# Optimization experiments

Hardware: AMD Instinct MI355X
Metric: run time of the kernel (lower is better)

The kernel has to match this reference:

```python
import jax, jax.numpy as jnp
import numpy as np

HIDDEN = 2048
N_HEADS = 16
N_KV = 4
HEAD_DIM = 128
SEQ = 2048
BATCH = 2
THETA = 10000.0


def rotate_half(x):
    half = x.shape[-1] // 2
    x1, x2 = x[..., :half], x[..., half:]
    return jnp.concatenate((-x2, x1), axis=-1)


def rope_cos_sin(seq_len, dim, theta, dtype):
    inv_freq = 1.0 / (theta ** (jnp.arange(0, dim, 2, dtype=jnp.float32) / dim))
    t = jnp.arange(seq_len, dtype=jnp.float32)
    freqs = jnp.einsum('i,j->ij', t, inv_freq)            # [S, dim/2]
    emb = jnp.concatenate((freqs, freqs), axis=-1)        # [S, dim]
    return jnp.cos(emb).astype(dtype), jnp.sin(emb).astype(dtype)


def setup_inputs() -> dict:
    key = jax.random.key(0)
    kx, kq, kk, kv, ko = jax.random.split(key, 5)
    s = 0.02
    return {
        'x':  jax.random.normal(kx, (BATCH, SEQ, HIDDEN), dtype=jnp.float32),
        'Wq': jax.random.normal(kq, (HIDDEN, N_HEADS * HEAD_DIM), dtype=jnp.float32) * s,
        'Wk': jax.random.normal(kk, (HIDDEN, N_KV * HEAD_DIM), dtype=jnp.float32) * s,
        'Wv': jax.random.normal(kv, (HIDDEN, N_KV * HEAD_DIM), dtype=jnp.float32) * s,
        'Wo': jax.random.normal(ko, (N_HEADS * HEAD_DIM, HIDDEN), dtype=jnp.float32) * s,
    }


def reference(x, Wq, Wk, Wv, Wo):
    B, S, _ = x.shape
    q = (x @ Wq).reshape(B, S, N_HEADS, HEAD_DIM)
    k = (x @ Wk).reshape(B, S, N_KV, HEAD_DIM)
    v = (x @ Wv).reshape(B, S, N_KV, HEAD_DIM)

    cos, sin = rope_cos_sin(S, HEAD_DIM, THETA, x.dtype)
    cos = cos[None, :, None, :]  # [1,S,1,D]
    sin = sin[None, :, None, :]
    q = q * cos + rotate_half(q) * sin
    k = k * cos + rotate_half(k) * sin

    repeat = N_HEADS // N_KV
    k = jnp.repeat(k, repeat, axis=2)  # repeat_interleave over heads
    v = jnp.repeat(v, repeat, axis=2)

    # [B,H,S,D]
    q = q.transpose(0, 2, 1, 3)
    k = k.transpose(0, 2, 1, 3)
    v = v.transpose(0, 2, 1, 3)

    scale = HEAD_DIM ** -0.5
    scores = jnp.einsum('bhqd,bhkd->bhqk', q, k) * scale
    causal = jnp.triu(jnp.full((S, S), -jnp.inf, dtype=scores.dtype), k=1)
    scores = scores + causal
    probs = jax.nn.softmax(scores, axis=-1)
    out = jnp.einsum('bhqk,bhkd->bhqd', probs, v)
    out = out.transpose(0, 2, 1, 3).reshape(B, S, N_HEADS * HEAD_DIM)
    return out @ Wo
```

## Files before the change

### kernel.cpp

```cpp
#include <hip/hip_runtime.h>
#include <hip/hip_bf16.h>
#include <math.h>

#define HIDDEN 2048
#define NHEADS 16
#define NKV 4
#define HD 128
#define SEQ 2048
#define BATCH 2
#define MTOT (BATCH*SEQ)
#define NQ (NHEADS*HD)
#define NKVD (NKV*HD)
#define NQKV (NQ + 2*NKVD)

typedef __attribute__((ext_vector_type(8))) short short8;
typedef __attribute__((ext_vector_type(4))) float float4v;

#if __has_builtin(__builtin_amdgcn_exp2f)
#define EXP2F __builtin_amdgcn_exp2f
#else
#define EXP2F exp2f
#endif
#define C1 0.1275174f

static __device__ __forceinline__ unsigned short f2bf(float f) {
  union { float f; unsigned int u; } v; v.f = f;
  unsigned int r = v.u + 0x7FFF + ((v.u >> 16) & 1);
  return (unsigned short)(r >> 16);
}
static __device__ __forceinline__ float bf2f(unsigned short h) {
  union { unsigned int u; float f; } v; v.u = ((unsigned int)h) << 16;
  return v.f;
}

static __device__ __forceinline__ void async16(const unsigned short* g, unsigned short* l) {
  __builtin_amdgcn_global_load_lds(
      (const __attribute__((address_space(1))) unsigned int*)g,
      (__attribute__((address_space(3))) unsigned int*)l, 16, 0, 0);
}

__global__ void cast_f32_bf16(const float* __restrict__ in,
                              unsigned short* __restrict__ out, int n) {
  int i = (blockIdx.x * blockDim.x + threadIdx.x) * 4;
  if (i < n) {
    float4 v = *(const float4*)(in + i);
    ushort4 o;
    o.x = f2bf(v.x); o.y = f2bf(v.y); o.z = f2bf(v.z); o.w = f2bf(v.w);
    *(ushort4*)(out + i) = o;
  }
}

__global__ void transpose_cast(const float* __restrict__ W,
                               unsigned short* __restrict__ Wt, int K, int N) {
  __shared__ float tile[32][33];
  int tn = blockIdx.x * 32;
  int tk = blockIdx.y * 32;
  int tx = threadIdx.x & 31;
  int ty = threadIdx.x >> 5;
  #pragma unroll
  for (int i = 0; i < 4; i++) {
    int k = tk + ty + i * 8;
    tile[ty + i * 8][tx] = W[(size_t)k * N + tn + tx];
  }
  __syncthreads();
  #pragma unroll
  for (int i = 0; i < 4; i++) {
    int n = tn + ty + i * 8;
    Wt[(size_t)n * K + tk + tx] = f2bf(tile[tx][ty + i * 8]);
  }
}

__global__ void rope_kernel(unsigned short* __restrict__ Qb, int nheads) {
  int idx = blockIdx.x * blockDim.x + threadIdx.x;
  int d = idx & 63;
  int hr = idx >> 6;
  int spos = (hr / nheads) % SEQ;
  size_t base = (size_t)hr * HD;
  float inv = exp2f((float)d * -0.2076205059304601f);
  float ang = (float)spos * inv;
  float sn, cs;
  sincosf(ang, &sn, &cs);
  float q1 = bf2f(Qb[base + d]);
  float q2 = bf2f(Qb[base + d + 64]);
  Qb[base + d]      = f2bf(q1 * cs - q2 * sn);
  Qb[base + d + 64] = f2bf(q2 * cs + q1 * sn);
}

__global__ __launch_bounds__(256) void gemm_qkv(
    const unsigned short* __restrict__ A,
    const unsigned short* __restrict__ Bt,
    unsigned short* __restrict__ Qb,
    unsigned short* __restrict__ Kb,
    unsigned short* __restrict__ Vt) {
  __shared__ unsigned short As0[128 * 32], Bs0[128 * 32];
  __shared__ unsigned short As1[128 * 32], Bs1[128 * 32];
  const int K = HIDDEN;
  int bm = blockIdx.y * 128, bn = blockIdx.x * 128;
  int tid = threadIdx.x, w = tid >> 6, lane = tid & 63;
  int wm = (w >> 1) * 64, wn = (w & 1) * 64;
  int m16 = lane & 15, quad = lane >> 4;
  int lrow = lane >> 2, lch = lane & 3;
  const unsigned short* Ag = A + (size_t)(bm + w * 32 + lrow) * K + lch * 8;
  const unsigned short* Bg = Bt + (size_t)(bn + w * 32 + lrow) * K + lch * 8;
  int woff = w * 1024;

  float4v acc[4][4];
  #pragma unroll
  for (int i = 0; i < 4; i++)
    #pragma unroll
    for (int j = 0; j < 4; j++) acc[i][j] = (float4v)0.0f;

  auto stage = [&](int k0, unsigned short* Asl, unsigned short* Bsl) {
    #pragma unroll
    for (int i = 0; i < 2; i++) {
      async16(Ag + (size_t)i * 16 * K + k0, Asl + woff + i * 512);
      async16(Bg + (size_t)i * 16 * K + k0, Bsl + woff + i * 512);
    }
  };
  auto compute = [&](const unsigned short* As, const unsigned short* Bs) {
    short8 af[4], bfr[4];
    #pragma unroll
    for (int i = 0; i < 4; i++)
      af[i] = *(const short8*)(&As[(wm + i * 16 + m16) * 32 + quad * 8]);
    #pragma unroll
    for (int j = 0; j < 4; j++)
      bfr[j] = *(const short8*)(&Bs[(wn + j * 16 + m16) * 32 + quad * 8]);
    #pragma unroll
    for (int i = 0; i < 4; i++)
      #pragma unroll
      for (int j = 0; j < 4; j++)
        acc[i][j] = __builtin_amdgcn_mfma_f32_16x16x32_bf16(af[i], bfr[j], acc[i][j], 0, 0, 0);
  };

  stage(0, As0, Bs0);
  for (int k0 = 0; k0 < K; k0 += 64) {
    __syncthreads();
    if (k0 + 32 < K) stage(k0 + 32, As1, Bs1);
    compute(As0, Bs0);
    __syncthreads();
    if (k0 + 64 < K) stage(k0 + 64, As0, Bs0);
    compute(As1, Bs1);
  }

  if (blockIdx.x < 16) {
    #pragma unroll
    for (int i = 0; i < 4; i++)
      #pragma unroll
      for (int j = 0; j < 4; j++)
        #pragma unroll
        for (int r = 0; r < 4; r++) {
          int row = bm + wm + i * 16 + quad * 4 + r;
          int col = bn + wn + j * 16 + m16;
          Qb[(size_t)row * NQ + col] = f2bf(acc[i][j][r]);
        }
  } else if (blockIdx.x < 20) {
    #pragma unroll
    for (int i = 0; i < 4; i++)
      #pragma unroll
      for (int j = 0; j < 4; j++)
        #pragma unroll
        for (int r = 0; r < 4; r++) {
          int row = bm + wm + i * 16 + quad * 4 + r;
          int col = bn - 2048 + wn + j * 16 + m16;
          Kb[(size_t)row * NKVD + col] = f2bf(acc[i][j][r]);
        }
  } else {
    #pragma unroll
    for (int i = 0; i < 4; i++)
      #pragma unroll
      for (int j = 0; j < 4; j++) {
        int f = bn - 2560 + wn + j * 16 + m16;
        int row0 = bm + wm + i * 16 + quad * 4;
        uint2 u;
        u.x = ((unsigned)f2bf(acc[i][j][1]) << 16) | f2bf(acc[i][j][0]);
        u.y = ((unsigned)f2bf(acc[i][j][3]) << 16) | f2bf(acc[i][j][2]);
        *(uint2*)(Vt + (size_t)f * MTOT + row0) = u;
      }
  }
}

__global__ __launch_bounds__(256) void gemm_o(
    const unsigned short* __restrict__ A,
    const unsigned short* __restrict__ Bt,
    float* __restrict__ C, int M, int N, int K) {
  __shared__ unsigned short As0[128 * 32], Bs0[128 * 32];
  __shared__ unsigned short As1[128 * 32], Bs1[128 * 32];
  int bm = blockIdx.y * 128, bn = blockIdx.x * 128;
  int tid = threadIdx.x, w = tid >> 6, lane = tid & 63;
  int wm = (w >> 1) * 64, wn = (w & 1) * 64;
  int m16 = lane & 15, quad = lane >> 4;
  int lrow = lane >> 2, lch = lane & 3;
  const unsigned short* Ag = A + (size_t)(bm + w * 32 + lrow) * K + lch * 8;
  const unsigned short* Bg = Bt + (size_t)(bn + w * 32 + lrow) * K + lch * 8;
  int woff = w * 1024;

  float4v acc[4][4];
  #pragma unroll
  for (int i = 0; i < 4; i++)
    #pragma unroll
    for (int j = 0; j < 4; j++) acc[i][j] = (float4v)0.0f;

  auto stage = [&](int k0, unsigned short* Asl, unsigned short* Bsl) {
    #pragma unroll
    for (int i = 0; i < 2; i++) {
      async16(Ag + (size_t)i * 16 * K + k0, Asl + woff + i * 512);
      async16(Bg + (size_t)i * 16 * K + k0, Bsl + woff + i * 512);
    }
  };
  auto compute = [&](const unsigned short* As, const unsigned short* Bs) {
    short8 af[4], bfr[4];
    #pragma unroll
    for (int i = 0; i < 4; i++)
      af[i] = *(const short8*)(&As[(wm + i * 16 + m16) * 32 + quad * 8]);
    #pragma unroll
    for (int j = 0; j < 4; j++)
      bfr[j] = *(const short8*)(&Bs[(wn + j * 16 + m16) * 32 + quad * 8]);
    #pragma unroll
    for (int i = 0; i < 4; i++)
      #pragma unroll
      for (int j = 0; j < 4; j++)
        acc[i][j] = __builtin_amdgcn_mfma_f32_16x16x32_bf16(af[i], bfr[j], acc[i][j], 0, 0, 0);
  };

  stage(0, As0, Bs0);
  for (int k0 = 0; k0 < K; k0 += 64) {
    __syncthreads();
    if (k0 + 32 < K) stage(k0 + 32, As1, Bs1);
    compute(As0, Bs0);
    __syncthreads();
    if (k0 + 64 < K) stage(k0 + 64, As0, Bs0);
    compute(As1, Bs1);
  }

  #pragma unroll
  for (int i = 0; i < 4; i++)
    #pragma unroll
    for (int j = 0; j < 4; j++)
      #pragma unroll
      for (int r = 0; r < 4; r++) {
        int row = bm + wm + i * 16 + quad * 4 + r;
        int col = bn + wn + j * 16 + m16;
        C[(size_t)row * N + col] = acc[i][j][r];
      }
}

#define FLASH_TILE(CUR, NXT)                                                  \
  {                                                                           \
    const int ktb = kt * 64;                                                  \
    __syncthreads();           \
    {                                                                         \
      const unsigned short* Vg = Vt + vgrow * (size_t)MTOT                    \
                                    + (size_t)b * SEQ + ktb + kcv * 32 + lch * 8; \
      unsigned short* Vl = Vs + kcv * 4096 + ipv * 512;                       \
      _Pragma("unroll")                                                       \
      for (int i = 0; i < 4; i++) async16(Vg + (size_t)i * 16 * MTOT, Vl + i * 512); \
    }                                                                         \
    const bool act = (ktb <= wqmax);                                          \
    float4v sacc[2][4];                                                       \
    if (act) {                                                                \
      _Pragma("unroll") for (int qs = 0; qs < 2; qs++)                        \
        _Pragma("unroll") for (int s4 = 0; s4 < 4; s4++) sacc[qs][s4] = (float4v)0.0f; \
      _Pragma("unroll")                                                       \
      for (int s4 = 0; s4 < 4; s4++)                                          \
        _Pragma("unroll")                                                     \
        for (int c = 0; c < 4; c++) {                                         \
          short8 kf = *(const short8*)(&CUR[c * 2048 + (s4 * 16 + m16) * 32 + quad * 8]); \
          sacc[0][s4] = __builtin_amdgcn_mfma_f32_16x16x32_bf16(kf, qf[0][c], sacc[0][s4], 0, 0, 0); \
          sacc[1][s4] = __builtin_amdgcn_mfma_f32_16x16x32_bf16(kf, qf[1][c], sacc[1][s4], 0, 0, 0); \
        }                                                                     \
    }                                                                         \
    if (kt < H) {                                                             \
      const unsigned short* Kg = Kp + (((size_t)b * SEQ + (kt + 1) * 64 + lrow) * NKV + kvh) * HD + w * 32 + lch * 8; \
      unsigned short* Kl = NXT + w * 2048;                                    \
      _Pragma("unroll")                                                       \
      for (int i = 0; i < 4; i++) async16(Kg + (size_t)i * 16 * NKV * HD, Kl + i * 512); \
    }                                                                         \
    if (act) {                                                                \
      _Pragma("unroll")                                                       \
      for (int qs = 0; qs < 2; qs++) {                                        \
        const int qabs = wqbase + qs * 16 + m16;                              \
        const bool diag = (ktb + 63) > (wqbase + qs * 16);                    \
        float sv[4][4]; float mloc = -1e30f;                                  \
        if (diag) {                                                           \
          _Pragma("unroll") for (int s4 = 0; s4 < 4; s4++)                    \
            _Pragma("unroll") for (int r = 0; r < 4; r++) {                   \
              int kabs = ktb + s4 * 16 + quad * 4 + r;                        \
              float t = sacc[qs][s4][r];                                      \
              sv[s4][r] = (kabs > qabs) ? -1e30f : t;                         \
              mloc = fmaxf(mloc, sv[s4][r]); }                                \
        } else {                                                              \
          _Pragma("unroll") for (int s4 = 0; s4 < 4; s4++)                    \
            _Pragma("unroll") for (int r = 0; r < 4; r++) {                   \
              sv[s4][r] = sacc[qs][s4][r]; mloc = fmaxf(mloc, sv[s4][r]); }   \
        }                                                                     \
        mloc *= C1;                                                           \
        mloc = fmaxf(mloc, __shfl_xor(mloc, 16, 64));                         \
        mloc = fmaxf(mloc, __shfl_xor(mloc, 32, 64));                         \
        const float mnewS = fmaxf(miS[qs], mloc);                             \
        float pr[4][4]; float rs = 0.0f;                                      \
        _Pragma("unroll") for (int s4 = 0; s4 < 4; s4++)                      \
          _Pragma("unroll") for (int r = 0; r < 4; r++) {                     \
            float p = EXP2F(__builtin_fmaf(sv[s4][r], C1, -mnewS));           \
            pr[s4][r] = p; rs += p; }                                         \
        rs += __shfl_xor(rs, 16, 64);                                         \
        rs += __shfl_xor(rs, 32, 64);                                         \
        const float alpha = EXP2F(miS[qs] - mnewS);                           \
        li[qs] = li[qs] * alpha + rs; miS[qs] = mnewS;                        \
        _Pragma("unroll") for (int ds = 0; ds < 8; ds++) oacc[ds][qs] *= alpha; \
        const int prow = qlocal0 + qs * 16 + m16;                             \
        const int psw = prow * 32; const int rx = prow & 7;                   \
        _Pragma("unroll") for (int s4 = 0; s4 < 4; s4++) {                    \
          uint2 u;                                                            \
          u.x = (__float_as_uint(pr[s4][1]) & 0xffff0000u) | (__float_as_uint(pr[s4][0]) >> 16); \
          u.y = (__float_as_uint(pr[s4][3]) & 0xffff0000u) | (__float_as_uint(pr[s4][2]) >> 16); \
          int chunkW = s4 * 2 + (quad >> 1);                                  \
          *(uint2*)(&Ps[psw + ((chunkW ^ rx) << 2) + (quad & 1) * 2]) = u;    \
        }                                                                     \
      }                                                                       \
    }                                                                         \
    __syncthreads();     \
    if (act) {                                                                \
      const int r0 = qlocal0 + m16, r1 = qlocal0 + 16 + m16;                  \
      _Pragma("unroll")                                                       \
      for (int kc = 0; kc < 2; kc++) {                                        \
        short8 pf0 = *(const short8*)(&Ps[r0 * 32 + (((kc * 4 + quad) ^ (r0 & 7)) << 2)]); \
        short8 pf1 = *(const short8*)(&Ps[r1 * 32 + (((kc * 4 + quad) ^ (r1 & 7)) << 2)]); \
        _Pragma("unroll")                                                     \
        for (int ds = 0; ds < 8; ds++) {                                      \
          short8 vf = *(const short8*)(&Vs[kc * 4096 + (ds * 16 + m16) * 32 + quad * 8]); \
          oacc[ds][0] = __builtin_amdgcn_mfma_f32_16x16x32_bf16(vf, pf0, oacc[ds][0], 0, 0, 0); \
          oacc[ds][1] = __builtin_amdgcn_mfma_f32_16x16x32_bf16(vf, pf1, oacc[ds][1], 0, 0, 0); \
        }                                                                     \
      }                                                                       \
    }                                                                         \
  }

__global__ __launch_bounds__(256, 2) void flash_attn(
    const unsigned short* __restrict__ Q,
    const unsigned short* __restrict__ Kp,
    const unsigned short* __restrict__ Vt,
    unsigned short* __restrict__ O) {
  __shared__ unsigned short Ks0[4 * 64 * 32];
  __shared__ unsigned short Ks1[4 * 64 * 32];
  __shared__ unsigned short Vs[2 * 128 * 32];
  __shared__ unsigned int   Ps[128 * 32];

  int bx = blockIdx.x;
  int h  = blockIdx.y;
  int b  = blockIdx.z;
  int kvh = h >> 2;
  int H = 31 - bx, L = bx;
  int tid = threadIdx.x;
  int w = tid >> 6, lane = tid & 63;
  int m16 = lane & 15, quad = lane >> 4;
  int lrow = lane >> 2, lch = lane & 3;

  int wqbase = (w < 2) ? (H * 64 + w * 32) : (L * 64 + (w - 2) * 32);
  int wqmax = wqbase + 31;
  int qlocal0 = w * 32;
  const int kcv = w >> 1, ipv = (w & 1) * 4;
  const size_t vgrow = (size_t)kvh * HD + ipv * 16 + lrow;

  short8 qf[2][4];
  #pragma unroll
  for (int qs = 0; qs < 2; qs++) {
    size_t qbase = (((size_t)b * SEQ + wqbase + qs * 16 + m16) * NHEADS + h) * HD;
    #pragma unroll
    for (int c = 0; c < 4; c++)
      qf[qs][c] = *(const short8*)(Q + qbase + c * 32 + quad * 8);
  }

  float4v oacc[8][2];
  #pragma unroll
  for (int ds = 0; ds < 8; ds++) { oacc[ds][0] = (float4v)0.0f; oacc[ds][1] = (float4v)0.0f; }
  float miS[2] = {-1e30f, -1e30f}, li[2] = {0.0f, 0.0f};

  {
    const unsigned short* Kg = Kp + (((size_t)b * SEQ + lrow) * NKV + kvh) * HD + w * 32 + lch * 8;
    unsigned short* Kl = Ks0 + w * 2048;
    #pragma unroll
    for (int i = 0; i < 4; i++) async16(Kg + (size_t)i * 16 * NKV * HD, Kl + i * 512);
  }

  int kt = 0;
  for (;;) {
    FLASH_TILE(Ks0, Ks1)
    if (++kt > H) break;
    FLASH_TILE(Ks1, Ks0)
    if (++kt > H) break;
  }

  #pragma unroll
  for (int qs = 0; qs < 2; qs++) {
    float inv = 1.0f / li[qs];
    int qabs = wqbase + qs * 16 + m16;
    size_t obase = (((size_t)b * SEQ + qabs) * NHEADS + h) * HD + quad * 4;
    #pragma unroll
    for (int ds = 0; ds < 8; ds++) {
      float v0 = oacc[ds][qs][0] * inv;
      float v1 = oacc[ds][qs][1] * inv;
      float v2 = oacc[ds][qs][2] * inv;
      float v3 = oacc[ds][qs][3] * inv;
      uint2 u;
      u.x = ((unsigned)f2bf(v1) << 16) | f2bf(v0);
      u.y = ((unsigned)f2bf(v3) << 16) | f2bf(v2);
      *(uint2*)(O + obase + ds * 16) = u;
    }
  }
}

extern "C" void kernel_launch(void* const* d_in, const int* in_sizes, int n_in,
                              void* d_out, int out_size, void* d_ws, size_t ws_size,
                              hipStream_t stream) {
  const float* x  = (const float*)d_in[0];
  const float* Wq = (const float*)d_in[1];
  const float* Wk = (const float*)d_in[2];
  const float* Wv = (const float*)d_in[3];
  const float* Wo = (const float*)d_in[4];
  float* out = (float*)d_out;

  unsigned short* ws = (unsigned short*)d_ws;
  unsigned short* xb  = ws;
  unsigned short* Wqt = xb  + (size_t)MTOT * HIDDEN;
  unsigned short* Wkt = Wqt + (size_t)NQ * HIDDEN;
  unsigned short* Wvt = Wkt + (size_t)NKVD * HIDDEN;
  unsigned short* Wot = Wvt + (size_t)NKVD * HIDDEN;
  unsigned short* Qb  = Wot + (size_t)NQ * HIDDEN;
  unsigned short* Kb  = Qb  + (size_t)MTOT * NQ;
  unsigned short* Vtb = Kb  + (size_t)MTOT * NKVD;
  unsigned short* Ab  = Vtb + (size_t)MTOT * NKVD;

  cast_f32_bf16<<<(MTOT * HIDDEN / 4 + 255) / 256, 256, 0, stream>>>(x, xb, MTOT * HIDDEN);
  transpose_cast<<<dim3(NQ / 32, HIDDEN / 32), 256, 0, stream>>>(Wq, Wqt, HIDDEN, NQ);
  transpose_cast<<<dim3(NKVD / 32, HIDDEN / 32), 256, 0, stream>>>(Wk, Wkt, HIDDEN, NKVD);
  transpose_cast<<<dim3(NKVD / 32, HIDDEN / 32), 256, 0, stream>>>(Wv, Wvt, HIDDEN, NKVD);
  transpose_cast<<<dim3(NQ / 32, HIDDEN / 32), 256, 0, stream>>>(Wo, Wot, NQ, HIDDEN);

  gemm_qkv<<<dim3(NQKV / 128, MTOT / 128), 256, 0, stream>>>(xb, Wqt, Qb, Kb, Vtb);

  rope_kernel<<<(BATCH * SEQ * NHEADS * 64) / 256, 256, 0, stream>>>(Qb, NHEADS);
  rope_kernel<<<(BATCH * SEQ * NKV * 64) / 256, 256, 0, stream>>>(Kb, NKV);

  flash_attn<<<dim3(16, NHEADS, BATCH), 256, 0, stream>>>(Qb, Kb, Vtb, Ab);

  gemm_o<<<dim3(HIDDEN / 128, MTOT / 128), 256, 0, stream>>>(Ab, Wot, out, MTOT, HIDDEN, NQ);
}
```

Before: 328.0 us.

## Swizzle LDS tiles, alias P buffer onto K tile, raise flash occupancy

Applies an XOR swizzle to the global-to-LDS chunk placement and to the fragment reads in both GEMMs and in the flash attention K/V tiles, aiming to reduce LDS bank conflicts. The flash kernel drops its separate P scratch buffer and writes P into the current K tile after an extra barrier, packing the probabilities into registers first; the lower LDS footprint allows launch bounds of 3 blocks per SM. The V projection swaps MFMA operand order so the transposed V store becomes a per-element scalar write. Risks include an extra barrier per tile, higher register pressure from the 3-block bound, and less coalesced V stores.

```diff
diff --git a/kernel.cpp b/kernel.cpp
--- a/kernel.cpp
+++ b/kernel.cpp
@@ -100,8 +100,10 @@
   int wm = (w >> 1) * 64, wn = (w & 1) * 64;
   int m16 = lane & 15, quad = lane >> 4;
   int lrow = lane >> 2, lch = lane & 3;
-  const unsigned short* Ag = A + (size_t)(bm + w * 32 + lrow) * K + lch * 8;
-  const unsigned short* Bg = Bt + (size_t)(bn + w * 32 + lrow) * K + lch * 8;
+  int lchs = lch ^ ((lrow >> 1) & 3);
+  int qx = quad ^ ((m16 >> 1) & 3);
+  const unsigned short* Ag = A + (size_t)(bm + w * 32 + lrow) * K + lchs * 8;
+  const unsigned short* Bg = Bt + (size_t)(bn + w * 32 + lrow) * K + lchs * 8;
   int woff = w * 1024;
 
   float4v acc[4][4];
@@ -117,29 +119,55 @@
       async16(Bg + (size_t)i * 16 * K + k0, Bsl + woff + i * 512);
     }
   };
-  auto compute = [&](const unsigned short* As, const unsigned short* Bs) {
+  auto computeN = [&](const unsigned short* As, const unsigned short* Bs) {
     short8 af[4], bfr[4];
     #pragma unroll
     for (int i = 0; i < 4; i++)
-      af[i] = *(const short8*)(&As[(wm + i * 16 + m16) * 32 + quad * 8]);
+      af[i] = *(const short8*)(&As[(wm + i * 16 + m16) * 32 + qx * 8]);
     #pragma unroll
     for (int j = 0; j < 4; j++)
-      bfr[j] = *(const short8*)(&Bs[(wn + j * 16 + m16) * 32 + quad * 8]);
+      bfr[j] = *(const short8*)(&Bs[(wn + j * 16 + m16) * 32 + qx * 8]);
     #pragma unroll
     for (int i = 0; i < 4; i++)
       #pragma unroll
       for (int j = 0; j < 4; j++)
         acc[i][j] = __builtin_amdgcn_mfma_f32_16x16x32_bf16(af[i], bfr[j], acc[i][j], 0, 0, 0);
   };
-
+  auto computeS = [&](const unsigned short* As, const unsigned short* Bs) {
+    short8 af[4], bfr[4];
+    #pragma unroll
+    for (int i = 0; i < 4; i++)
+      af[i] = *(const short8*)(&As[(wm + i * 16 + m16) * 32 + qx * 8]);
+    #pragma unroll
+    for (int j = 0; j < 4; j++)
+      bfr[j] = *(const short8*)(&Bs[(wn + j * 16 + m16) * 32 + qx * 8]);
+    #pragma unroll
+    for (int i = 0; i < 4; i++)
+      #pragma unroll
+      for (int j = 0; j < 4; j++)
+        acc[i][j] = __builtin_amdgcn_mfma_f32_16x16x32_bf16(bfr[j], af[i], acc[i][j], 0, 0, 0);
+  };
+
+  bool isV = (blockIdx.x >= 20);
   stage(0, As0, Bs0);
-  for (int k0 = 0; k0 < K; k0 += 64) {
-    __syncthreads();
-    if (k0 + 32 < K) stage(k0 + 32, As1, Bs1);
-    compute(As0, Bs0);
-    __syncthreads();
-    if (k0 + 64 < K) stage(k0 + 64, As0, Bs0);
-    compute(As1, Bs1);
+  if (!isV) {
+    for (int k0 = 0; k0 < K; k0 += 64) {
+      __syncthreads();
+      if (k0 + 32 < K) stage(k0 + 32, As1, Bs1);
+      computeN(As0, Bs0);
+      __syncthreads();
+      if (k0 + 64 < K) stage(k0 + 64, As0, Bs0);
+      computeN(As1, Bs1);
+    }
+  } else {
+    for (int k0 = 0; k0 < K; k0 += 64) {
+      __syncthreads();
+      if (k0 + 32 < K) stage(k0 + 32, As1, Bs1);
+      computeS(As0, Bs0);
+      __syncthreads();
+      if (k0 + 64 < K) stage(k0 + 64, As0, Bs0);
+      computeS(As1, Bs1);
+    }
   }
 
   if (blockIdx.x < 16) {
@@ -153,7 +181,7 @@
           int col = bn + wn + j * 16 + m16;
           Qb[(size_t)row * NQ + col] = f2bf(acc[i][j][r]);
         }
-  } else if (blockIdx.x < 20) {
+  } else if (!isV) {
     #pragma unroll
     for (int i = 0; i < 4; i++)
       #pragma unroll
@@ -168,14 +196,13 @@
     #pragma unroll
     for (int i = 0; i < 4; i++)
       #pragma unroll
-      for (int j = 0; j < 4; j++) {
-        int f = bn - 2560 + wn + j * 16 + m16;
-        int row0 = bm + wm + i * 16 + quad * 4;
-        uint2 u;
-        u.x = ((unsigned)f2bf(acc[i][j][1]) << 16) | f2bf(acc[i][j][0]);
-        u.y = ((unsigned)f2bf(acc[i][j][3]) << 16) | f2bf(acc[i][j][2]);
-        *(uint2*)(Vt + (size_t)f * MTOT + row0) = u;
-      }
+      for (int j = 0; j < 4; j++)
+        #pragma unroll
+        for (int r = 0; r < 4; r++) {
+          int f = bn - 2560 + wn + j * 16 + quad * 4 + r;
+          int m = bm + wm + i * 16 + m16;
+          Vt[(size_t)f * MTOT + m] = f2bf(acc[i][j][r]);
+        }
   }
 }
 
@@ -190,8 +217,10 @@
   int wm = (w >> 1) * 64, wn = (w & 1) * 64;
   int m16 = lane & 15, quad = lane >> 4;
   int lrow = lane >> 2, lch = lane & 3;
-  const unsigned short* Ag = A + (size_t)(bm + w * 32 + lrow) * K + lch * 8;
-  const unsigned short* Bg = Bt + (size_t)(bn + w * 32 + lrow) * K + lch * 8;
+  int lchs = lch ^ ((lrow >> 1) & 3);
+  int qx = quad ^ ((m16 >> 1) & 3);
+  const unsigned short* Ag = A + (size_t)(bm + w * 32 + lrow) * K + lchs * 8;
+  const unsigned short* Bg = Bt + (size_t)(bn + w * 32 + lrow) * K + lchs * 8;
   int woff = w * 1024;
 
   float4v acc[4][4];
@@ -211,10 +240,10 @@
     short8 af[4], bfr[4];
     #pragma unroll
     for (int i = 0; i < 4; i++)
-      af[i] = *(const short8*)(&As[(wm + i * 16 + m16) * 32 + quad * 8]);
+      af[i] = *(const short8*)(&As[(wm + i * 16 + m16) * 32 + qx * 8]);
     #pragma unroll
     for (int j = 0; j < 4; j++)
-      bfr[j] = *(const short8*)(&Bs[(wn + j * 16 + m16) * 32 + quad * 8]);
+      bfr[j] = *(const short8*)(&Bs[(wn + j * 16 + m16) * 32 + qx * 8]);
     #pragma unroll
     for (int i = 0; i < 4; i++)
       #pragma unroll
@@ -247,10 +276,10 @@
 #define FLASH_TILE(CUR, NXT)                                                  \
   {                                                                           \
     const int ktb = kt * 64;                                                  \
-    __syncthreads();           \
+    __syncthreads();                                                 \
     {                                                                         \
       const unsigned short* Vg = Vt + vgrow * (size_t)MTOT                    \
-                                    + (size_t)b * SEQ + ktb + kcv * 32 + lch * 8; \
+                                    + (size_t)b * SEQ + ktb + kcv * 32 + vlch * 8; \
       unsigned short* Vl = Vs + kcv * 4096 + ipv * 512;                       \
       _Pragma("unroll")                                                       \
       for (int i = 0; i < 4; i++) async16(Vg + (size_t)i * 16 * MTOT, Vl + i * 512); \
@@ -264,17 +293,18 @@
       for (int s4 = 0; s4 < 4; s4++)                                          \
         _Pragma("unroll")                                                     \
         for (int c = 0; c < 4; c++) {                                         \
-          short8 kf = *(const short8*)(&CUR[c * 2048 + (s4 * 16 + m16) * 32 + quad * 8]); \
+          short8 kf = *(const short8*)(&CUR[c * 2048 + (s4 * 16 + m16) * 32 + qx * 8]); \
           sacc[0][s4] = __builtin_amdgcn_mfma_f32_16x16x32_bf16(kf, qf[0][c], sacc[0][s4], 0, 0, 0); \
           sacc[1][s4] = __builtin_amdgcn_mfma_f32_16x16x32_bf16(kf, qf[1][c], sacc[1][s4], 0, 0, 0); \
         }                                                                     \
     }                                                                         \
     if (kt < H) {                                                             \
-      const unsigned short* Kg = Kp + (((size_t)b * SEQ + (kt + 1) * 64 + lrow) * NKV + kvh) * HD + w * 32 + lch * 8; \
+      const unsigned short* Kg = Kp + (((size_t)b * SEQ + (kt + 1) * 64 + lrow) * NKV + kvh) * HD + w * 32 + vlch * 8; \
       unsigned short* Kl = NXT + w * 2048;                                    \
       _Pragma("unroll")                                                       \
       for (int i = 0; i < 4; i++) async16(Kg + (size_t)i * 16 * NKV * HD, Kl + i * 512); \
     }                                                                         \
+    unsigned int pu[2][4][2];                                                 \
     if (act) {                                                                \
       _Pragma("unroll")                                                       \
       for (int qs = 0; qs < 2; qs++) {                                        \
@@ -297,37 +327,44 @@
         mloc = fmaxf(mloc, __shfl_xor(mloc, 16, 64));                         \
         mloc = fmaxf(mloc, __shfl_xor(mloc, 32, 64));                         \
         const float mnewS = fmaxf(miS[qs], mloc);                             \
-        float pr[4][4]; float rs = 0.0f;                                      \
-        _Pragma("unroll") for (int s4 = 0; s4 < 4; s4++)                      \
-          _Pragma("unroll") for (int r = 0; r < 4; r++) {                     \
-            float p = EXP2F(__builtin_fmaf(sv[s4][r], C1, -mnewS));           \
-            pr[s4][r] = p; rs += p; }                                         \
+        float rs = 0.0f;                                                      \
+        _Pragma("unroll") for (int s4 = 0; s4 < 4; s4++) {                    \
+          float p0 = EXP2F(__builtin_fmaf(sv[s4][0], C1, -mnewS));            \
+          float p1 = EXP2F(__builtin_fmaf(sv[s4][1], C1, -mnewS));            \
+          float p2 = EXP2F(__builtin_fmaf(sv[s4][2], C1, -mnewS));            \
+          float p3 = EXP2F(__builtin_fmaf(sv[s4][3], C1, -mnewS));            \
+          rs += p0 + p1 + p2 + p3;                                            \
+          pu[qs][s4][0] = (__float_as_uint(p1) & 0xffff0000u) | (__float_as_uint(p0) >> 16); \
+          pu[qs][s4][1] = (__float_as_uint(p3) & 0xffff0000u) | (__float_as_uint(p2) >> 16); \
+        }                                                                     \
         rs += __shfl_xor(rs, 16, 64);                                         \
         rs += __shfl_xor(rs, 32, 64);                                         \
         const float alpha = EXP2F(miS[qs] - mnewS);                           \
         li[qs] = li[qs] * alpha + rs; miS[qs] = mnewS;                        \
         _Pragma("unroll") for (int ds = 0; ds < 8; ds++) oacc[ds][qs] *= alpha; \
+      }                                                                       \
+    }                                                                         \
+    __syncthreads();  \
+    if (act) {                                                                \
+      unsigned int* Pp = (unsigned int*)CUR;                                  \
+      _Pragma("unroll")                                                       \
+      for (int qs = 0; qs < 2; qs++) {                                        \
         const int prow = qlocal0 + qs * 16 + m16;                             \
         const int psw = prow * 32; const int rx = prow & 7;                   \
         _Pragma("unroll") for (int s4 = 0; s4 < 4; s4++) {                    \
-          uint2 u;                                                            \
-          u.x = (__float_as_uint(pr[s4][1]) & 0xffff0000u) | (__float_as_uint(pr[s4][0]) >> 16); \
-          u.y = (__float_as_uint(pr[s4][3]) & 0xffff0000u) | (__float_as_uint(pr[s4][2]) >> 16); \
+          uint2 u; u.x = pu[qs][s4][0]; u.y = pu[qs][s4][1];                  \
           int chunkW = s4 * 2 + (quad >> 1);                                  \
-          *(uint2*)(&Ps[psw + ((chunkW ^ rx) << 2) + (quad & 1) * 2]) = u;    \
+          *(uint2*)(&Pp[psw + ((chunkW ^ rx) << 2) + (quad & 1) * 2]) = u;    \
         }                                                                     \
       }                                                                       \
-    }                                                                         \
-    __syncthreads();     \
-    if (act) {                                                                \
       const int r0 = qlocal0 + m16, r1 = qlocal0 + 16 + m16;                  \
       _Pragma("unroll")                                                       \
       for (int kc = 0; kc < 2; kc++) {                                        \
-        short8 pf0 = *(const short8*)(&Ps[r0 * 32 + (((kc * 4 + quad) ^ (r0 & 7)) << 2)]); \
-        short8 pf1 = *(const short8*)(&Ps[r1 * 32 + (((kc * 4 + quad) ^ (r1 & 7)) << 2)]); \
+        short8 pf0 = *(const short8*)(&Pp[r0 * 32 + (((kc * 4 + quad) ^ (r0 & 7)) << 2)]); \
+        short8 pf1 = *(const short8*)(&Pp[r1 * 32 + (((kc * 4 + quad) ^ (r1 & 7)) << 2)]); \
         _Pragma("unroll")                                                     \
         for (int ds = 0; ds < 8; ds++) {                                      \
-          short8 vf = *(const short8*)(&Vs[kc * 4096 + (ds * 16 + m16) * 32 + quad * 8]); \
+          short8 vf = *(const short8*)(&Vs[kc * 4096 + (ds * 16 + m16) * 32 + qx * 8]); \
           oacc[ds][0] = __builtin_amdgcn_mfma_f32_16x16x32_bf16(vf, pf0, oacc[ds][0], 0, 0, 0); \
           oacc[ds][1] = __builtin_amdgcn_mfma_f32_16x16x32_bf16(vf, pf1, oacc[ds][1], 0, 0, 0); \
         }                                                                     \
@@ -335,7 +372,7 @@
     }                                                                         \
   }
 
-__global__ __launch_bounds__(256, 2) void flash_attn(
+__global__ __launch_bounds__(256, 3) void flash_attn(
     const unsigned short* __restrict__ Q,
     const unsigned short* __restrict__ Kp,
     const unsigned short* __restrict__ Vt,
@@ -343,7 +380,6 @@
   __shared__ unsigned short Ks0[4 * 64 * 32];
   __shared__ unsigned short Ks1[4 * 64 * 32];
   __shared__ unsigned short Vs[2 * 128 * 32];
-  __shared__ unsigned int   Ps[128 * 32];
 
   int bx = blockIdx.x;
   int h  = blockIdx.y;
@@ -354,6 +390,8 @@
   int w = tid >> 6, lane = tid & 63;
   int m16 = lane & 15, quad = lane >> 4;
   int lrow = lane >> 2, lch = lane & 3;
+  const int vlch = lch ^ ((lrow >> 1) & 3);
+  const int qx = quad ^ ((m16 >> 1) & 3);
 
   int wqbase = (w < 2) ? (H * 64 + w * 32) : (L * 64 + (w - 2) * 32);
   int wqmax = wqbase + 31;
@@ -376,7 +414,7 @@
   float miS[2] = {-1e30f, -1e30f}, li[2] = {0.0f, 0.0f};
 
   {
-    const unsigned short* Kg = Kp + (((size_t)b * SEQ + lrow) * NKV + kvh) * HD + w * 32 + lch * 8;
+    const unsigned short* Kg = Kp + (((size_t)b * SEQ + lrow) * NKV + kvh) * HD + w * 32 + vlch * 8;
     unsigned short* Kl = Ks0 + w * 2048;
     #pragma unroll
     for (int i = 0; i < 4; i++) async16(Kg + (size_t)i * 16 * NKV * HD, Kl + i * 512);
```

Measured after the change: 540.5 us. 1.65x slower.
